# Kernel optimization log

Measured on AMD Instinct MI355X. Metric: run time of the kernel, lower is better.

Reference implementation:

```python
import jax, jax.numpy as jnp
import numpy as np

HALF = 32          # (input_dim-1)//2
HIDDEN = 128
OUT_DIM = 10
B, T, C = 256, 512, 65


def setup_inputs() -> dict:
    key = jax.random.key(0)
    ks = jax.random.split(key, 20)
    s = 0.05
    gin = HALF + HIDDEN
    inp = {
        "times": jnp.arange(T, dtype=jnp.float32),
        "coeff_a": jax.random.normal(ks[0], (B, T - 1, C), jnp.float32),
        "coeff_b": jax.random.normal(ks[1], (B, T - 1, C), jnp.float32),
        "coeff_two_c": jax.random.normal(ks[2], (B, T - 1, C), jnp.float32),
        "coeff_three_d": jax.random.normal(ks[3], (B, T - 1, C), jnp.float32),
        "final_index": jax.random.randint(ks[4], (B,), 0, T),
        "Wr": jax.random.normal(ks[5], (gin, HIDDEN), jnp.float32) * s,
        "br": jnp.zeros((HIDDEN,), jnp.float32),
        "Wz": jax.random.normal(ks[6], (gin, HIDDEN), jnp.float32) * s,
        "bz": jnp.zeros((HIDDEN,), jnp.float32),
        "Wxn": jax.random.normal(ks[7], (HALF, HIDDEN), jnp.float32) * s,
        "bxn": jnp.zeros((HIDDEN,), jnp.float32),
        "Whn": jax.random.normal(ks[8], (HIDDEN, HIDDEN), jnp.float32) * s,
        "bhn": jnp.zeros((HIDDEN,), jnp.float32),
        "W_ode": jax.random.normal(ks[9], (HIDDEN, HIDDEN), jnp.float32) * s,
        "b_ode": jnp.zeros((HIDDEN,), jnp.float32),
        "W_lin": jax.random.normal(ks[10], (HIDDEN, OUT_DIM), jnp.float32) * s,
        "b_lin": jnp.zeros((OUT_DIM,), jnp.float32),
    }
    return inp


def _forward(times, coeff_a, coeff_b, coeff_two_c, coeff_three_d, final_index,
             Wr, br, Wz, bz, Wxn, bxn, Whn, bhn, W_ode, b_ode, W_lin, b_lin):
    maxlen = coeff_b.shape[-2] - 1

    def eval_spline(t):
        idx = jnp.clip(jnp.sum(t > times) - 1, 0, maxlen)
        fr = t - times[idx]
        inner = 0.5 * coeff_two_c[:, idx, :] + coeff_three_d[:, idx, :] * (fr / 3.0)
        inner = coeff_b[:, idx, :] + inner * fr
        return coeff_a[:, idx, :] + inner * fr  # [B, C]

    X = jax.vmap(eval_spline, out_axes=1)(times)  # [B, T, C]
    # difference the observation-indicator channels over time; make channel 0 a time delta
    X = X.at[:, 1:, 1:1 + HALF].add(-X[:, :-1, 1:1 + HALF])
    X = X.at[:, 0, 0].add(-times[0])
    X = X.at[:, 1:, 0].add(-times[:-1])

    nbatch = X.shape[0]

    def gru(x, h):
        comb = jnp.concatenate([x, h], axis=1)
        r = jax.nn.sigmoid(comb @ Wr + br)
        z = jax.nn.sigmoid(comb @ Wz + bz)
        n = jnp.tanh(x @ Wxn + bxn + (h @ Whn + bhn) * r)
        return (1.0 - z) * n + z * h

    def f_ode(h):
        return jnp.tanh(h @ W_ode + b_ode)

    def evolve(h, td):
        # single RK4 step from 0 to td
        k1 = f_ode(h)
        k2 = f_ode(h + 0.5 * td * k1)
        k3 = f_ode(h + 0.5 * td * k2)
        k4 = f_ode(h + td * k3)
        return h + (td / 6.0) * (k1 + 2.0 * k2 + 2.0 * k3 + k4)

    def step(h, dt, Xi):
        obs = jnp.max(Xi[:, 1:1 + HALF], axis=1) > 0.5
        Xp = Xi[:, 1 + HALF:].at[:, 0].add(dt)
        new_h = gru(Xp, h)

        def take(hd):
            h0, dt0 = hd
            return (jnp.where(obs[:, None], new_h, h0),
                    dt0 + jnp.where(obs, 0.0, Xi[:, 0]))

        return jax.lax.cond(jnp.any(obs), take, lambda hd: hd, (h, dt))

    z0 = jnp.zeros((nbatch, HIDDEN), X.dtype)
    dt0 = jnp.zeros((nbatch,), X.dtype)
    h0, dt0 = step(z0, dt0, X[:, 0])

    time_diffs = times[1:] - times[:-1]
    Xs = jnp.moveaxis(X[:, 1:], 1, 0)  # [T-1, B, C]

    def scan_body(carry, inp):
        h, dt = carry
        td, Xi = inp
        h = evolve(h, td)
        h, dt = step(h, dt, Xi)
        return (h, dt), h

    _, hs_rest = jax.lax.scan(scan_body, (h0, dt0), (time_diffs, Xs))
    out = jnp.concatenate([h0[:, None], jnp.moveaxis(hs_rest, 0, 1)], axis=1)  # [B, T, H]
    final = out[jnp.arange(nbatch), final_index]  # [B, H]
    return final @ W_lin + b_lin


def reference(times, coeff_a, coeff_b, coeff_two_c, coeff_three_d, final_index,
              Wr, br, Wz, bz, Wxn, bxn, Whn, bhn, W_ode, b_ode, W_lin, b_lin):
    return _forward(times, coeff_a, coeff_b, coeff_two_c, coeff_three_d, final_index,
                    Wr, br, Wz, bz, Wxn, bxn, Whn, bhn, W_ode, b_ode, W_lin, b_lin)
```

## Files before the change

kernel.cpp:

```cpp
#include <hip/hip_runtime.h>

#define TT 512
#define BB 256
#define CC 65
#define HALFC 32
#define HID 128
#define ODIM 10

__device__ __forceinline__ float ftanh(float x) {
  float u = __builtin_amdgcn_exp2f(x * -2.885390082f);
  return fmaf(2.f, __builtin_amdgcn_rcpf(1.f + u), -1.f);
}
__device__ __forceinline__ float fsig(float x) {
  float u = __builtin_amdgcn_exp2f(x * -1.442695041f);
  return __builtin_amdgcn_rcpf(1.f + u);
}

template <int CTRL>
__device__ __forceinline__ float dpp_add(float x) {
  return x + __int_as_float(__builtin_amdgcn_update_dpp(
      0, __float_as_int(x), CTRL, 0xF, 0xF, true));
}
__device__ __forceinline__ float red8(float x) {
  x = dpp_add<0x101>(x);
  x = dpp_add<0x102>(x);
  x = dpp_add<0x104>(x);
  return x;
}

__device__ __forceinline__ void block_sync_lds() {
  asm volatile("s_waitcnt lgkmcnt(0)" ::: "memory");
  __builtin_amdgcn_s_barrier();
  asm volatile("" ::: "memory");
}
__device__ __forceinline__ void vm_wait0() {
  asm volatile("s_waitcnt vmcnt(0)" ::: "memory");
}

__device__ __forceinline__ int permf4(int f) { return ((f & 3) << 3) | (f >> 2); }
__device__ __forceinline__ int slot_byteoff(int s) {
  return permf4(s >> 1) * 16 + (s & 1) * 8;
}

__global__ void prep0(const float* __restrict__ times, float4* __restrict__ si,
                      int* __restrict__ anyobs) {
  __shared__ float ts[TT];
  int t = threadIdx.x;
  ts[t] = times[t];
  __syncthreads();
  float tv = ts[t];
  int cnt = 0;
  for (int jj = 0; jj < TT; ++jj) cnt += (tv > ts[jj]) ? 1 : 0;
  int idx = cnt - 1;
  idx = min(max(idx, 0), TT - 2);
  float4 o;
  o.x = __int_as_float(idx);
  o.y = tv - ts[idx];
  o.z = (t == 0) ? 0.f : (tv - ts[t - 1]);
  o.w = (t == 0) ? ts[0] : ts[t - 1];
  si[t] = o;
  anyobs[t] = 0;
}

__global__ void prep_obs(const float* __restrict__ ca, const float* __restrict__ cb,
                         const float* __restrict__ cc2, const float* __restrict__ cd,
                         const float4* __restrict__ si, int* __restrict__ anyobs,
                         unsigned char* __restrict__ obs) {
  int grp = blockIdx.x * (blockDim.x >> 5) + (threadIdx.x >> 5);
  int lane = threadIdx.x & 31;
  int t = grp & (TT - 1);
  int b = grp / TT;
  int ch = 1 + lane;
  float4 s = si[t];
  int idx = __float_as_int(s.x);
  float fr = s.y;
  size_t base = ((size_t)b * (TT - 1) + idx) * CC + ch;
  float f3 = fr / 3.f;
  float v = ca[base] + (cb[base] + (0.5f * cc2[base] + cd[base] * f3) * fr) * fr;
  float D = v;
  if (t >= 1) {
    float4 sp = si[t - 1];
    int idxp = __float_as_int(sp.x);
    float frp = sp.y;
    size_t basep = ((size_t)b * (TT - 1) + idxp) * CC + ch;
    float f3p = frp / 3.f;
    float vp = ca[basep] + (cb[basep] + (0.5f * cc2[basep] + cd[basep] * f3p) * frp) * frp;
    D = v - vp;
  }
  float m = D;
  #pragma unroll
  for (int off = 16; off >= 1; off >>= 1) m = fmaxf(m, __shfl_xor(m, off));
  if (lane == 0) {
    unsigned char o = (m > 0.5f) ? (unsigned char)1 : (unsigned char)0;
    obs[(size_t)b * TT + t] = o;
    if (o) atomicOr(&anyobs[t], 1);
  }
}

__launch_bounds__(512, 2)
__global__ void ode_main(
    const float* __restrict__ ca, const float* __restrict__ cb,
    const float* __restrict__ cc2, const float* __restrict__ cd,
    const int* __restrict__ final_index,
    const float* __restrict__ Wr, const float* __restrict__ br,
    const float* __restrict__ Wz, const float* __restrict__ bz,
    const float* __restrict__ Wxn, const float* __restrict__ bxn,
    const float* __restrict__ Whn, const float* __restrict__ bhn,
    const float* __restrict__ Wode, const float* __restrict__ bode,
    const float* __restrict__ Wlin, const float* __restrict__ blin,
    const float4* __restrict__ si, const int* __restrict__ anyobs,
    const unsigned char* __restrict__ obsArr,
    float* __restrict__ out)
{
  __shared__ alignas(16) float hS[HID];
  __shared__ alignas(16) float vA[HID];
  __shared__ alignas(16) float vB[HID];
  __shared__ alignas(16) float xs[HALFC];
  __shared__ alignas(16) float4 siL[TT];
  __shared__ unsigned char flagL[TT];

  const int tid = threadIdx.x;
  const int b = blockIdx.x;
  const int lane = tid & 63;
  const int wv = tid >> 6;
  const int jslot = lane >> 3;
  const int kk = lane & 7;
  const int j0 = wv * 16 + jslot * 2;
  const int wroff = slot_byteoff(wv * 8 + jslot);

  float wode[32], whn[32], wrh[32], wzh[32];
  float wrx[8], wzx[8], wxn[8];
  #pragma unroll
  for (int i = 0; i < 16; ++i) {
    const int row = 16 * kk + i;
    float2 q;
    q = *(const float2*)&Wode[row * HID + j0]; wode[2*i] = q.x; wode[2*i+1] = q.y;
    q = *(const float2*)&Whn [row * HID + j0]; whn [2*i] = q.x; whn [2*i+1] = q.y;
    q = *(const float2*)&Wr[(HALFC + row) * HID + j0]; wrh[2*i] = q.x; wrh[2*i+1] = q.y;
    q = *(const float2*)&Wz[(HALFC + row) * HID + j0]; wzh[2*i] = q.x; wzh[2*i+1] = q.y;
  }
  #pragma unroll
  for (int i = 0; i < 4; ++i) {
    const int xrow = 4 * kk + i;
    float2 q;
    q = *(const float2*)&Wr [xrow * HID + j0]; wrx[2*i] = q.x; wrx[2*i+1] = q.y;
    q = *(const float2*)&Wz [xrow * HID + j0]; wzx[2*i] = q.x; wzx[2*i+1] = q.y;
    q = *(const float2*)&Wxn[xrow * HID + j0]; wxn[2*i] = q.x; wxn[2*i+1] = q.y;
  }
  float bo0, bo1, bh0, bh1, br0, br1, bz0, bz1, bx0, bx1;
  { float2 q;
    q = *(const float2*)&bode[j0]; bo0 = q.x; bo1 = q.y;
    q = *(const float2*)&bhn [j0]; bh0 = q.x; bh1 = q.y;
    q = *(const float2*)&br  [j0]; br0 = q.x; br1 = q.y;
    q = *(const float2*)&bz  [j0]; bz0 = q.x; bz1 = q.y;
    q = *(const float2*)&bxn [j0]; bx0 = q.x; bx1 = q.y;
  }
  const int fidx = final_index[b];

  {
    siL[tid] = si[tid];
    const int ao = anyobs[tid];
    const unsigned char o = obsArr[(size_t)b * TT + tid];
    flagL[tid] = (unsigned char)((ao ? 1 : 0) | (o ? 2 : 0));
  }
  if (tid < HID) { hS[tid] = 0.f; vA[tid] = 0.f; vB[tid] = 0.f; }
  if (tid < HALFC) xs[tid] = 0.f;
  float hj0 = 0.f, hj1 = 0.f;
  float dtv = 0.f;
  block_sync_lds();

  auto mv = [&](const float* __restrict__ buf, const float (&w)[32],
                float& o0, float& o1) {
    const float4* b4 = (const float4*)buf;
    float vv[16];
    #pragma unroll
    for (int q = 0; q < 4; ++q) {
      const float4 x4 = b4[q * 8 + kk];
      vv[4*q] = x4.x; vv[4*q+1] = x4.y; vv[4*q+2] = x4.z; vv[4*q+3] = x4.w;
    }
    float a0 = 0.f, a1 = 0.f;
    #pragma unroll
    for (int i = 0; i < 16; ++i) {
      a0 = fmaf(vv[i], w[2*i],   a0);
      a1 = fmaf(vv[i], w[2*i+1], a1);
    }
    o0 = red8(a0); o1 = red8(a1);
  };

  float4 s = siL[0];
  int flg = flagL[0];

  for (int t = 0; ; ++t) {
    const int sidx = __float_as_int(s.x);
    const float fr = s.y, td = s.z, tsub = s.w;
    const bool apply = (flg & 1) && (flg & 2);

    float xa = 0.f, xb = 0.f, xc = 0.f, xd = 0.f;
    float ya = 0.f, yb = 0.f, yc = 0.f, yd = 0.f;
    if (tid < 32) {
      const size_t base = ((size_t)b * (TT - 1) + sidx) * CC;
      const int ch = 33 + tid;
      xa = ca[base + ch]; xb = cb[base + ch]; xc = cc2[base + ch]; xd = cd[base + ch];
      if (tid == 0) { ya = ca[base]; yb = cb[base]; yc = cc2[base]; yd = cd[base]; }
    }

    if (t > 0) {
      const float htd = 0.5f * td;
      float p0, p1, k0, k1, ks0, ks1;
      mv(hS, wode, p0, p1);
      k0 = ftanh(p0 + bo0); k1 = ftanh(p1 + bo1);
      ks0 = k0; ks1 = k1;
      if (kk == 0)
        *(float2*)((char*)vA + wroff) =
            make_float2(fmaf(htd, k0, hj0), fmaf(htd, k1, hj1));
      block_sync_lds();
      mv(vA, wode, p0, p1);
      k0 = ftanh(p0 + bo0); k1 = ftanh(p1 + bo1);
      ks0 = fmaf(2.f, k0, ks0); ks1 = fmaf(2.f, k1, ks1);
      if (kk == 0)
        *(float2*)((char*)vB + wroff) =
            make_float2(fmaf(htd, k0, hj0), fmaf(htd, k1, hj1));
      block_sync_lds();
      mv(vB, wode, p0, p1);
      k0 = ftanh(p0 + bo0); k1 = ftanh(p1 + bo1);
      ks0 = fmaf(2.f, k0, ks0); ks1 = fmaf(2.f, k1, ks1);
      if (kk == 0)
        *(float2*)((char*)vA + wroff) =
            make_float2(fmaf(td, k0, hj0), fmaf(td, k1, hj1));
      block_sync_lds();
      mv(vA, wode, p0, p1);
      k0 = ftanh(p0 + bo0); k1 = ftanh(p1 + bo1);
      ks0 += k0; ks1 += k1;
      hj0 = fmaf(td * (1.f / 6.f), ks0, hj0);
      hj1 = fmaf(td * (1.f / 6.f), ks1, hj1);
      if (kk == 0)
        *(float2*)((char*)vB + wroff) = make_float2(hj0, hj1);
    }

    float xdelta = 0.f;
    vm_wait0();
    if (tid < 32) {
      const float f3 = fr * (1.f / 3.f);
      float sv = xa + (xb + (0.5f * xc + xd * f3) * fr) * fr;
      if (tid == 0) {
        const float s0 = ya + (yb + (0.5f * yc + yd * f3) * fr) * fr;
        xdelta = s0 - tsub;
        sv += dtv;
      }
      xs[tid] = sv;
    }
    block_sync_lds();

    {
      const float4* b4 = (const float4*)vB;
      float vv[16];
      #pragma unroll
      for (int q = 0; q < 4; ++q) {
        const float4 x4 = b4[q * 8 + kk];
        vv[4*q] = x4.x; vv[4*q+1] = x4.y; vv[4*q+2] = x4.z; vv[4*q+3] = x4.w;
      }
      float rp0 = 0.f, rp1 = 0.f, zp0 = 0.f, zp1 = 0.f;
      float gp0 = 0.f, gp1 = 0.f, xp0 = 0.f, xp1 = 0.f;
      #pragma unroll
      for (int i = 0; i < 16; ++i) {
        rp0 = fmaf(vv[i], wrh[2*i],   rp0); rp1 = fmaf(vv[i], wrh[2*i+1], rp1);
        zp0 = fmaf(vv[i], wzh[2*i],   zp0); zp1 = fmaf(vv[i], wzh[2*i+1], zp1);
        gp0 = fmaf(vv[i], whn[2*i],   gp0); gp1 = fmaf(vv[i], whn[2*i+1], gp1);
      }
      const float4 xq = ((const float4*)xs)[kk];
      const float xv[4] = {xq.x, xq.y, xq.z, xq.w};
      #pragma unroll
      for (int i = 0; i < 4; ++i) {
        rp0 = fmaf(xv[i], wrx[2*i],   rp0); rp1 = fmaf(xv[i], wrx[2*i+1], rp1);
        zp0 = fmaf(xv[i], wzx[2*i],   zp0); zp1 = fmaf(xv[i], wzx[2*i+1], zp1);
        xp0 = fmaf(xv[i], wxn[2*i],   xp0); xp1 = fmaf(xv[i], wxn[2*i+1], xp1);
      }
      rp0 = red8(rp0); rp1 = red8(rp1);
      zp0 = red8(zp0); zp1 = red8(zp1);
      gp0 = red8(gp0); gp1 = red8(gp1);
      xp0 = red8(xp0); xp1 = red8(xp1);
      const float r0 = fsig(rp0 + br0), r1 = fsig(rp1 + br1);
      const float z0 = fsig(zp0 + bz0), z1 = fsig(zp1 + bz1);
      const float n0 = ftanh(xp0 + bx0 + (gp0 + bh0) * r0);
      const float n1 = ftanh(xp1 + bx1 + (gp1 + bh1) * r1);
      const float h0n = fmaf(z0, hj0 - n0, n0);
      const float h1n = fmaf(z1, hj1 - n1, n1);
      hj0 = apply ? h0n : hj0;
      hj1 = apply ? h1n : hj1;
      if (kk == 0)
        *(float2*)((char*)hS + wroff) = make_float2(hj0, hj1);
    }
    if (tid == 0 && (flg & 1) && !(flg & 2)) dtv += xdelta;

    if (t == fidx) break;
    const int tn = t + 1;
    s = siL[tn];
    flg = flagL[tn];
    block_sync_lds();
  }

  block_sync_lds();
  if (tid < ODIM) {
    float acc = blin[tid];
    const float* hf = (const float*)hS;
    #pragma unroll 8
    for (int q = 0; q < HID; ++q) {
      const float hv = hf[permf4(q >> 2) * 4 + (q & 3)];
      acc = fmaf(hv, Wlin[q * ODIM + tid], acc);
    }
    out[b * ODIM + tid] = acc;
  }
}

extern "C" void kernel_launch(void* const* d_in, const int* in_sizes, int n_in,
                              void* d_out, int out_size, void* d_ws, size_t ws_size,
                              hipStream_t stream) {
  const float* times = (const float*)d_in[0];
  const float* ca   = (const float*)d_in[1];
  const float* cb   = (const float*)d_in[2];
  const float* cc2  = (const float*)d_in[3];
  const float* cd   = (const float*)d_in[4];
  const int*   fidx = (const int*)d_in[5];
  const float* Wr   = (const float*)d_in[6];
  const float* br   = (const float*)d_in[7];
  const float* Wz   = (const float*)d_in[8];
  const float* bz   = (const float*)d_in[9];
  const float* Wxn  = (const float*)d_in[10];
  const float* bxn  = (const float*)d_in[11];
  const float* Whn  = (const float*)d_in[12];
  const float* bhn  = (const float*)d_in[13];
  const float* Wode = (const float*)d_in[14];
  const float* bode = (const float*)d_in[15];
  const float* Wlin = (const float*)d_in[16];
  const float* blin = (const float*)d_in[17];
  float* out = (float*)d_out;

  char* ws = (char*)d_ws;
  float4* si = (float4*)ws;
  int* anyobs = (int*)(ws + TT * 16);
  unsigned char* obs = (unsigned char*)(ws + TT * 16 + TT * 4);

  prep0<<<1, TT, 0, stream>>>(times, si, anyobs);
  prep_obs<<<(BB * TT) / 8, 256, 0, stream>>>(ca, cb, cc2, cd, si, anyobs, obs);
  ode_main<<<BB, 512, 0, stream>>>(ca, cb, cc2, cd, fidx, Wr, br, Wz, bz,
                                   Wxn, bxn, Whn, bhn, Wode, bode, Wlin, blin,
                                   si, anyobs, obs, out);
}
```

Before: 1.101 ms.

## Double threads per block to shorten per-thread recurrent matvec chains

Launches the sequential ODE-GRU kernel with 1024 threads per batch row instead of 512. Each output pair is now reduced across 16 lanes rather than 8, so each thread holds half as many weights and runs half as many FMAs per step. This is meant to shorten the serial per-timestep latency of the recurrence. In exchange it adds one more DPP reduction stage, uses more waves per block for barriers, and puts more pressure on occupancy. The hidden-state reads now go through the permuted layout index.

```diff
diff --git a/kernel.cpp b/kernel.cpp
--- a/kernel.cpp
+++ b/kernel.cpp
@@ -21,10 +21,11 @@
   return x + __int_as_float(__builtin_amdgcn_update_dpp(
       0, __float_as_int(x), CTRL, 0xF, 0xF, true));
 }
-__device__ __forceinline__ float red8(float x) {
+__device__ __forceinline__ float red16(float x) {
   x = dpp_add<0x101>(x);
   x = dpp_add<0x102>(x);
   x = dpp_add<0x104>(x);
+  x = dpp_add<0x108>(x);
   return x;
 }
 
@@ -97,7 +98,7 @@
   }
 }
 
-__launch_bounds__(512, 2)
+__launch_bounds__(1024, 4)
 __global__ void ode_main(
     const float* __restrict__ ca, const float* __restrict__ cb,
     const float* __restrict__ cc2, const float* __restrict__ cd,
@@ -123,29 +124,28 @@
   const int b = blockIdx.x;
   const int lane = tid & 63;
   const int wv = tid >> 6;
-  const int jslot = lane >> 3;
-  const int kk = lane & 7;
-  const int j0 = wv * 16 + jslot * 2;
-  const int wroff = slot_byteoff(wv * 8 + jslot);
-
-  float wode[32], whn[32], wrh[32], wzh[32];
-  float wrx[8], wzx[8], wxn[8];
+  const int jslot = lane >> 4;
+  const int kk = lane & 15;
+  const int spair = wv * 4 + jslot;
+  const int j0 = 2 * spair;
+  const int wroff = slot_byteoff(spair);
+
+  float2 wode[8], whn[8], wrh[8], wzh[8];
+  float2 wrx[2], wzx[2], wxn[2];
   #pragma unroll
-  for (int i = 0; i < 16; ++i) {
-    const int row = 16 * kk + i;
-    float2 q;
-    q = *(const float2*)&Wode[row * HID + j0]; wode[2*i] = q.x; wode[2*i+1] = q.y;
-    q = *(const float2*)&Whn [row * HID + j0]; whn [2*i] = q.x; whn [2*i+1] = q.y;
-    q = *(const float2*)&Wr[(HALFC + row) * HID + j0]; wrh[2*i] = q.x; wrh[2*i+1] = q.y;
-    q = *(const float2*)&Wz[(HALFC + row) * HID + j0]; wzh[2*i] = q.x; wzh[2*i+1] = q.y;
+  for (int i = 0; i < 8; ++i) {
+    const int row = 8 * kk + i;
+    wode[i] = *(const float2*)&Wode[row * HID + j0];
+    whn [i] = *(const float2*)&Whn [row * HID + j0];
+    wrh [i] = *(const float2*)&Wr[(HALFC + row) * HID + j0];
+    wzh [i] = *(const float2*)&Wz[(HALFC + row) * HID + j0];
   }
   #pragma unroll
-  for (int i = 0; i < 4; ++i) {
-    const int xrow = 4 * kk + i;
-    float2 q;
-    q = *(const float2*)&Wr [xrow * HID + j0]; wrx[2*i] = q.x; wrx[2*i+1] = q.y;
-    q = *(const float2*)&Wz [xrow * HID + j0]; wzx[2*i] = q.x; wzx[2*i+1] = q.y;
-    q = *(const float2*)&Wxn[xrow * HID + j0]; wxn[2*i] = q.x; wxn[2*i+1] = q.y;
+  for (int i = 0; i < 2; ++i) {
+    const int xrow = 2 * kk + i;
+    wrx[i] = *(const float2*)&Wr [xrow * HID + j0];
+    wzx[i] = *(const float2*)&Wz [xrow * HID + j0];
+    wxn[i] = *(const float2*)&Wxn[xrow * HID + j0];
   }
   float bo0, bo1, bh0, bh1, br0, br1, bz0, bz1, bx0, bx1;
   { float2 q;
@@ -157,7 +157,7 @@
   }
   const int fidx = final_index[b];
 
-  {
+  if (tid < TT) {
     siL[tid] = si[tid];
     const int ao = anyobs[tid];
     const unsigned char o = obsArr[(size_t)b * TT + tid];
@@ -169,22 +169,20 @@
   float dtv = 0.f;
   block_sync_lds();
 
-  auto mv = [&](const float* __restrict__ buf, const float (&w)[32],
+  auto mv = [&](const float* __restrict__ buf, const float2 (&w)[8],
                 float& o0, float& o1) {
     const float4* b4 = (const float4*)buf;
-    float vv[16];
-    #pragma unroll
-    for (int q = 0; q < 4; ++q) {
-      const float4 x4 = b4[q * 8 + kk];
-      vv[4*q] = x4.x; vv[4*q+1] = x4.y; vv[4*q+2] = x4.z; vv[4*q+3] = x4.w;
-    }
+    const float4 A = b4[permf4(2 * kk)];
+    const float4 B4 = b4[permf4(2 * kk + 1)];
+    const float vv[8] = {A.x, A.y, A.z, A.w, B4.x, B4.y, B4.z, B4.w};
     float a0 = 0.f, a1 = 0.f;
     #pragma unroll
-    for (int i = 0; i < 16; ++i) {
-      a0 = fmaf(vv[i], w[2*i],   a0);
-      a1 = fmaf(vv[i], w[2*i+1], a1);
-    }
-    o0 = red8(a0); o1 = red8(a1);
+    for (int i = 0; i < 8; ++i) {
+      a0 = fmaf(vv[i], w[i].x, a0);
+      a1 = fmaf(vv[i], w[i].y, a1);
+    }
+    o0 = red16(a0);
+    o1 = red16(a1);
   };
 
   float4 s = siL[0];
@@ -253,32 +251,28 @@
 
     {
       const float4* b4 = (const float4*)vB;
-      float vv[16];
-      #pragma unroll
-      for (int q = 0; q < 4; ++q) {
-        const float4 x4 = b4[q * 8 + kk];
-        vv[4*q] = x4.x; vv[4*q+1] = x4.y; vv[4*q+2] = x4.z; vv[4*q+3] = x4.w;
-      }
+      const float4 A = b4[permf4(2 * kk)];
+      const float4 B4 = b4[permf4(2 * kk + 1)];
+      const float vv[8] = {A.x, A.y, A.z, A.w, B4.x, B4.y, B4.z, B4.w};
       float rp0 = 0.f, rp1 = 0.f, zp0 = 0.f, zp1 = 0.f;
       float gp0 = 0.f, gp1 = 0.f, xp0 = 0.f, xp1 = 0.f;
       #pragma unroll
-      for (int i = 0; i < 16; ++i) {
-        rp0 = fmaf(vv[i], wrh[2*i],   rp0); rp1 = fmaf(vv[i], wrh[2*i+1], rp1);
-        zp0 = fmaf(vv[i], wzh[2*i],   zp0); zp1 = fmaf(vv[i], wzh[2*i+1], zp1);
-        gp0 = fmaf(vv[i], whn[2*i],   gp0); gp1 = fmaf(vv[i], whn[2*i+1], gp1);
+      for (int i = 0; i < 8; ++i) {
+        rp0 = fmaf(vv[i], wrh[i].x, rp0); rp1 = fmaf(vv[i], wrh[i].y, rp1);
+        zp0 = fmaf(vv[i], wzh[i].x, zp0); zp1 = fmaf(vv[i], wzh[i].y, zp1);
+        gp0 = fmaf(vv[i], whn[i].x, gp0); gp1 = fmaf(vv[i], whn[i].y, gp1);
       }
-      const float4 xq = ((const float4*)xs)[kk];
-      const float xv[4] = {xq.x, xq.y, xq.z, xq.w};
-      #pragma unroll
-      for (int i = 0; i < 4; ++i) {
-        rp0 = fmaf(xv[i], wrx[2*i],   rp0); rp1 = fmaf(xv[i], wrx[2*i+1], rp1);
-        zp0 = fmaf(xv[i], wzx[2*i],   zp0); zp1 = fmaf(xv[i], wzx[2*i+1], zp1);
-        xp0 = fmaf(xv[i], wxn[2*i],   xp0); xp1 = fmaf(xv[i], wxn[2*i+1], xp1);
-      }
-      rp0 = red8(rp0); rp1 = red8(rp1);
-      zp0 = red8(zp0); zp1 = red8(zp1);
-      gp0 = red8(gp0); gp1 = red8(gp1);
-      xp0 = red8(xp0); xp1 = red8(xp1);
+      const float2 xv = ((const float2*)xs)[kk];
+      rp0 = fmaf(xv.x, wrx[0].x, fmaf(xv.y, wrx[1].x, rp0));
+      rp1 = fmaf(xv.x, wrx[0].y, fmaf(xv.y, wrx[1].y, rp1));
+      zp0 = fmaf(xv.x, wzx[0].x, fmaf(xv.y, wzx[1].x, zp0));
+      zp1 = fmaf(xv.x, wzx[0].y, fmaf(xv.y, wzx[1].y, zp1));
+      xp0 = fmaf(xv.x, wxn[0].x, fmaf(xv.y, wxn[1].x, xp0));
+      xp1 = fmaf(xv.x, wxn[0].y, fmaf(xv.y, wxn[1].y, xp1));
+      rp0 = red16(rp0); rp1 = red16(rp1);
+      zp0 = red16(zp0); zp1 = red16(zp1);
+      gp0 = red16(gp0); gp1 = red16(gp1);
+      xp0 = red16(xp0); xp1 = red16(xp1);
       const float r0 = fsig(rp0 + br0), r1 = fsig(rp1 + br1);
       const float z0 = fsig(zp0 + bz0), z1 = fsig(zp1 + bz1);
       const float n0 = ftanh(xp0 + bx0 + (gp0 + bh0) * r0);
@@ -342,7 +336,7 @@
 
   prep0<<<1, TT, 0, stream>>>(times, si, anyobs);
   prep_obs<<<(BB * TT) / 8, 256, 0, stream>>>(ca, cb, cc2, cd, si, anyobs, obs);
-  ode_main<<<BB, 512, 0, stream>>>(ca, cb, cc2, cd, fidx, Wr, br, Wz, bz,
-                                   Wxn, bxn, Whn, bhn, Wode, bode, Wlin, blin,
-                                   si, anyobs, obs, out);
-}
+  ode_main<<<BB, 1024, 0, stream>>>(ca, cb, cc2, cd, fidx, Wr, br, Wz, bz,
+                                    Wxn, bxn, Whn, bhn, Wode, bode, Wlin, blin,
+                                    si, anyobs, obs, out);
+}
```

Measured after the change: 1.332 ms. 1.21x slower.
